# Performance work log

Measured on AMD Instinct MI355X. Metric: run time of the kernel, lower is better.

The kernel has to match this reference:

```python
import jax, jax.numpy as jnp
import numpy as np

NUM_EMB = 256
EMB_DIM = 128
COMMIT_COST = 0.25


def setup_inputs() -> dict:
    key = jax.random.key(0)
    k1, k2 = jax.random.split(key)
    z = jax.random.normal(k1, (64, EMB_DIM, 64, 64), dtype=jnp.float32)
    # codebook initialized uniform(-1/num_embeddings, 1/num_embeddings)
    emb = jax.random.uniform(k2, (NUM_EMB, EMB_DIM), dtype=jnp.float32,
                             minval=-1.0 / NUM_EMB, maxval=1.0 / NUM_EMB)
    return {"z": z, "emb": emb}


def reference(z, emb):
    B, C, H, W = z.shape
    # [B, C, H, W] -> [B*H*W, C]
    z_flat = jnp.transpose(z, (0, 2, 3, 1)).reshape(-1, C)
    # squared L2 distances to each code: ||z||^2 - 2 z.e + ||e||^2, shape [N, K]
    d = (jnp.sum(z_flat * z_flat, axis=1, keepdims=True)
         - 2.0 * jnp.einsum('nc,kc->nk', z_flat, emb)
         + jnp.sum(emb * emb, axis=1))
    idx = jnp.argmin(d, axis=1)  # [N]
    # gather codes, back to NCHW
    quantized = emb[idx].reshape(B, H, W, C)
    quantized = jnp.transpose(quantized, (0, 3, 1, 2))
    commitment_loss = COMMIT_COST * jnp.mean(
        (jax.lax.stop_gradient(quantized) - z) ** 2)
    codebook_loss = jnp.mean((quantized - jax.lax.stop_gradient(z)) ** 2)
    # straight-through estimator
    quantized_ste = z + jax.lax.stop_gradient(quantized - z)
    return (quantized_ste, idx.reshape(B, H, W), commitment_loss, codebook_loss)
```

## Files before the change

kernel.cpp:

```cpp
#include <hip/hip_runtime.h>

#define K_EMB   256
#define C_DIM   128
#define HW      4096
#define NPOS    262144
#define Q_ELEMS 33554432
#define IDX_OFF Q_ELEMS
#define LOSS_OFF (Q_ELEMS + NPOS)

#define BLKP 64
#define TK   32
#define NQ   8
#define NTHR 512

#define WS_ENORM 0
#define WS_ACC   256
#define WS_EMBT  512
#define WS_NEED_FULL  ((WS_EMBT + C_DIM * K_EMB) * 4)

__global__ __launch_bounds__(K_EMB) void vq_transpose(const float* __restrict__ emb,
                                                      float* __restrict__ ws,
                                                      int use_embT) {
    const int c = blockIdx.x, k = threadIdx.x;
    if (use_embT) ws[WS_EMBT + c * K_EMB + k] = emb[k * C_DIM + c];
    if (c == 0 && k == 0) ws[WS_ACC] = 0.f;
}

__global__ __launch_bounds__(K_EMB) void vq_enorm(const float* __restrict__ emb,
                                                  float* __restrict__ ws) {
    const int k = threadIdx.x;
    const float4* __restrict__ er = reinterpret_cast<const float4*>(emb + k * C_DIM);
    float s = 0.f;
    #pragma unroll
    for (int j = 0; j < C_DIM / 4; ++j) {
        float4 v = er[j];
        s = fmaf(v.x, v.x, s);
        s = fmaf(v.y, v.y, s);
        s = fmaf(v.z, v.z, s);
        s = fmaf(v.w, v.w, s);
    }
    ws[WS_ENORM + k] = s;
}

template <int UT>
__global__ __launch_bounds__(NTHR, 4) void vq_main(const float* __restrict__ z,
                                                   const float* __restrict__ emb,
                                                   const float* __restrict__ ws,
                                                   float* __restrict__ out,
                                                   float* __restrict__ loss_acc) {
    __shared__ float zlds[C_DIM * BLKP];
    __shared__ float sh_best[NQ * BLKP];
    __shared__ int   sh_bidx[NQ * BLKP];

    const int t    = threadIdx.x;
    const int lane = t & 63;
    const int kq   = t >> 6;
    const int blk  = blockIdx.x;
    const int b    = blk >> 6;
    const int hw0  = (blk & 63) * BLKP;
    const size_t zoff = (size_t)b * (C_DIM * HW) + hw0;
    const float* __restrict__ zsrc = z + zoff;

    {
        const float4* __restrict__ zs4 = reinterpret_cast<const float4*>(zsrc);
        float4* __restrict__ zl4 = reinterpret_cast<float4*>(zlds);
        #pragma unroll
        for (int j = 0; j < (C_DIM * BLKP / 4) / NTHR; ++j) {
            const int i4 = t + j * NTHR;
            const int c  = i4 >> 4;
            const int p4 = i4 & 15;
            zl4[i4] = zs4[(size_t)c * (HW / 4) + p4];
        }
    }
    __syncthreads();

    const float* __restrict__ embT  = ws + WS_EMBT;
    const float* __restrict__ enorm = ws + WS_ENORM;

    const int kbase = __builtin_amdgcn_readfirstlane(kq * TK);

    float acc[TK];
    #pragma unroll
    for (int j = 0; j < TK; ++j) acc[j] = 0.f;
    float znorm = 0.f;

    #pragma unroll 2
    for (int c = 0; c < C_DIM; ++c) {
        const float zc = zlds[c * BLKP + lane];
        znorm = fmaf(zc, zc, znorm);
        if (UT) {
            const float* __restrict__ ep = embT + c * K_EMB + kbase;
            #pragma unroll
            for (int j = 0; j < TK; ++j)
                acc[j] = fmaf(zc, ep[j], acc[j]);
        } else {
            #pragma unroll
            for (int j = 0; j < TK; ++j)
                acc[j] = fmaf(zc, emb[(kbase + j) * C_DIM + c], acc[j]);
        }
    }

    float best = 3.402823466e38f;
    int   bidx = 0;
    #pragma unroll
    for (int j = 0; j < TK; ++j) {
        const float d = (znorm - 2.0f * acc[j]) + enorm[kbase + j];
        if (d < best) { best = d; bidx = kbase + j; }
    }

    sh_best[t] = best;
    sh_bidx[t] = bidx;
    __syncthreads();

    if (t < BLKP) {
        const int p = t;
        float bb = sh_best[p];
        int   bi = sh_bidx[p];
        #pragma unroll
        for (int q = 1; q < NQ; ++q) {
            const float bq = sh_best[q * BLKP + p];
            const int   iq = sh_bidx[q * BLKP + p];
            if (bq < bb) { bb = bq; bi = iq; }
        }
        const int fin = bi;
        const int pos = blk * BLKP + p;
        __builtin_nontemporal_store((float)fin, &out[IDX_OFF + pos]);

        float lsum = 0.f;
        float* qp = out + zoff + p;
        const float4* __restrict__ er =
            reinterpret_cast<const float4*>(emb + fin * C_DIM);
        #pragma unroll 4
        for (int j = 0; j < C_DIM / 4; ++j) {
            const float4 ev = er[j];
            const int c0 = j * 4;
            const float z0 = zlds[(c0 + 0) * BLKP + p];
            const float z1 = zlds[(c0 + 1) * BLKP + p];
            const float z2 = zlds[(c0 + 2) * BLKP + p];
            const float z3 = zlds[(c0 + 3) * BLKP + p];
            const float d0 = ev.x - z0, d1 = ev.y - z1;
            const float d2 = ev.z - z2, d3 = ev.w - z3;
            lsum = fmaf(d0, d0, lsum);
            lsum = fmaf(d1, d1, lsum);
            lsum = fmaf(d2, d2, lsum);
            lsum = fmaf(d3, d3, lsum);
            __builtin_nontemporal_store(z0 + d0, &qp[(size_t)(c0 + 0) * HW]);
            __builtin_nontemporal_store(z1 + d1, &qp[(size_t)(c0 + 1) * HW]);
            __builtin_nontemporal_store(z2 + d2, &qp[(size_t)(c0 + 2) * HW]);
            __builtin_nontemporal_store(z3 + d3, &qp[(size_t)(c0 + 3) * HW]);
        }

        #pragma unroll
        for (int off = 32; off > 0; off >>= 1)
            lsum += __shfl_down(lsum, off, 64);
        if (p == 0) atomicAdd(loss_acc, lsum);
    }
}

__global__ void vq_finalize(const float* __restrict__ loss_acc,
                            float* __restrict__ out_losses) {
    float S = loss_acc[0];
    float mean = S / (float)Q_ELEMS;
    out_losses[0] = 0.25f * mean;
    out_losses[1] = mean;
}

extern "C" void kernel_launch(void* const* d_in, const int* in_sizes, int n_in,
                              void* d_out, int out_size, void* d_ws, size_t ws_size,
                              hipStream_t stream) {
    const float* z   = (const float*)d_in[0];
    const float* emb = (const float*)d_in[1];
    float* out = (float*)d_out;
    float* ws  = (float*)d_ws;

    int use_embT = (ws_size >= (size_t)WS_NEED_FULL) ? 1 : 0;

    vq_transpose<<<C_DIM, K_EMB, 0, stream>>>(emb, ws, use_embT);
    vq_enorm<<<1, K_EMB, 0, stream>>>(emb, ws);
    if (use_embT)
        vq_main<1><<<NPOS / BLKP, NTHR, 0, stream>>>(z, emb, ws, out, ws + WS_ACC);
    else
        vq_main<0><<<NPOS / BLKP, NTHR, 0, stream>>>(z, emb, ws, out, ws + WS_ACC);
    vq_finalize<<<1, 1, 0, stream>>>(ws + WS_ACC, out + LOSS_OFF);
}
```

Before: 391.1 us.

## Register-tile distance GEMM as 4x8 position-by-code blocks with LDS argmin reduction

Replaces the one-position-per-thread, 32-codes-per-thread layout with a 4 positions × 8 codes register tile per thread. Each thread now does float4 LDS reads of z and float4 global reads of the transposed codebook, so every loaded value feeds more FMAs. The z norm is computed once per position by 64 threads instead of redundantly in the inner loop, and the code norms are staged in LDS. Partial argmins from 32 code groups go through LDS with packed byte indices and are reduced there. This adds an extra barrier and a longer final reduction loop (32 groups instead of 8).

```diff
diff --git a/kernel.cpp b/kernel.cpp
--- a/kernel.cpp
+++ b/kernel.cpp
@@ -9,9 +9,10 @@
 #define LOSS_OFF (Q_ELEMS + NPOS)
 
 #define BLKP 64
-#define TK   32
-#define NQ   8
 #define NTHR 512
+#define TM   4
+#define TN   8
+#define NKG  32
 
 #define WS_ENORM 0
 #define WS_ACC   256
@@ -49,17 +50,24 @@
                                                    float* __restrict__ out,
                                                    float* __restrict__ loss_acc) {
     __shared__ float zlds[C_DIM * BLKP];
-    __shared__ float sh_best[NQ * BLKP];
-    __shared__ int   sh_bidx[NQ * BLKP];
-
-    const int t    = threadIdx.x;
-    const int lane = t & 63;
-    const int kq   = t >> 6;
-    const int blk  = blockIdx.x;
-    const int b    = blk >> 6;
-    const int hw0  = (blk & 63) * BLKP;
+    __shared__ float shz[BLKP];
+    __shared__ float shen[K_EMB];
+    __shared__ float shpb[NKG * BLKP];
+    __shared__ unsigned int shpi[NKG * BLKP / 4];
+
+    const int t   = threadIdx.x;
+    const int pg  = t & 15;
+    const int p0  = pg * 4;
+    const int kg  = t >> 4;
+    const int k0  = kg * TN;
+    const int blk = blockIdx.x;
+    const int b   = blk >> 6;
+    const int hw0 = (blk & 63) * BLKP;
     const size_t zoff = (size_t)b * (C_DIM * HW) + hw0;
     const float* __restrict__ zsrc = z + zoff;
+
+    const float* __restrict__ embT    = ws + WS_EMBT;
+    const float* __restrict__ enorm_g = ws + WS_ENORM;
 
     {
         const float4* __restrict__ zs4 = reinterpret_cast<const float4*>(zsrc);
@@ -71,55 +79,80 @@
             const int p4 = i4 & 15;
             zl4[i4] = zs4[(size_t)c * (HW / 4) + p4];
         }
+        if (t < K_EMB) shen[t] = enorm_g[t];
     }
     __syncthreads();
 
-    const float* __restrict__ embT  = ws + WS_EMBT;
-    const float* __restrict__ enorm = ws + WS_ENORM;
-
-    const int kbase = __builtin_amdgcn_readfirstlane(kq * TK);
-
-    float acc[TK];
+    if (t < BLKP) {
+        float zn = 0.f;
+        #pragma unroll 8
+        for (int c = 0; c < C_DIM; ++c) {
+            const float zc = zlds[c * BLKP + t];
+            zn = fmaf(zc, zc, zn);
+        }
+        shz[t] = zn;
+    }
+
+    float acc[TM][TN];
     #pragma unroll
-    for (int j = 0; j < TK; ++j) acc[j] = 0.f;
-    float znorm = 0.f;
-
-    #pragma unroll 2
+    for (int i = 0; i < TM; ++i)
+        #pragma unroll
+        for (int j = 0; j < TN; ++j) acc[i][j] = 0.f;
+
+    #pragma unroll 4
     for (int c = 0; c < C_DIM; ++c) {
-        const float zc = zlds[c * BLKP + lane];
-        znorm = fmaf(zc, zc, znorm);
+        const float4 zv = *reinterpret_cast<const float4*>(&zlds[c * BLKP + p0]);
+        float ev[TN];
         if (UT) {
-            const float* __restrict__ ep = embT + c * K_EMB + kbase;
-            #pragma unroll
-            for (int j = 0; j < TK; ++j)
-                acc[j] = fmaf(zc, ep[j], acc[j]);
+            const float4* __restrict__ ep =
+                reinterpret_cast<const float4*>(embT + c * K_EMB + k0);
+            const float4 e0 = ep[0];
+            const float4 e1 = ep[1];
+            ev[0] = e0.x; ev[1] = e0.y; ev[2] = e0.z; ev[3] = e0.w;
+            ev[4] = e1.x; ev[5] = e1.y; ev[6] = e1.z; ev[7] = e1.w;
         } else {
             #pragma unroll
-            for (int j = 0; j < TK; ++j)
-                acc[j] = fmaf(zc, emb[(kbase + j) * C_DIM + c], acc[j]);
-        }
-    }
-
-    float best = 3.402823466e38f;
-    int   bidx = 0;
-    #pragma unroll
-    for (int j = 0; j < TK; ++j) {
-        const float d = (znorm - 2.0f * acc[j]) + enorm[kbase + j];
-        if (d < best) { best = d; bidx = kbase + j; }
-    }
-
-    sh_best[t] = best;
-    sh_bidx[t] = bidx;
+            for (int j = 0; j < TN; ++j) ev[j] = emb[(k0 + j) * C_DIM + c];
+        }
+        const float zz[TM] = {zv.x, zv.y, zv.z, zv.w};
+        #pragma unroll
+        for (int i = 0; i < TM; ++i)
+            #pragma unroll
+            for (int j = 0; j < TN; ++j)
+                acc[i][j] = fmaf(zz[i], ev[j], acc[i][j]);
+    }
+    __syncthreads();
+
+    {
+        float pb[TM];
+        int   pi[TM];
+        #pragma unroll
+        for (int i = 0; i < TM; ++i) {
+            const float zn = shz[p0 + i];
+            float best = 3.402823466e38f;
+            int   bi = 0;
+            #pragma unroll
+            for (int j = 0; j < TN; ++j) {
+                const float d = (zn - 2.0f * acc[i][j]) + shen[k0 + j];
+                if (d < best) { best = d; bi = k0 + j; }
+            }
+            pb[i] = best; pi[i] = bi;
+        }
+        *reinterpret_cast<float4*>(&shpb[kg * BLKP + p0]) =
+            make_float4(pb[0], pb[1], pb[2], pb[3]);
+        shpi[kg * 16 + pg] = (unsigned)(pi[0] & 255) | ((unsigned)(pi[1] & 255) << 8)
+                           | ((unsigned)(pi[2] & 255) << 16) | ((unsigned)(pi[3] & 255) << 24);
+    }
     __syncthreads();
 
     if (t < BLKP) {
         const int p = t;
-        float bb = sh_best[p];
-        int   bi = sh_bidx[p];
-        #pragma unroll
-        for (int q = 1; q < NQ; ++q) {
-            const float bq = sh_best[q * BLKP + p];
-            const int   iq = sh_bidx[q * BLKP + p];
+        float bb = shpb[p];
+        int   bi = (shpi[p >> 2] >> ((p & 3) * 8)) & 255;
+        #pragma unroll 4
+        for (int g = 1; g < NKG; ++g) {
+            const float bq = shpb[g * BLKP + p];
+            const int   iq = (shpi[g * 16 + (p >> 2)] >> ((p & 3) * 8)) & 255;
             if (bq < bb) { bb = bq; bi = iq; }
         }
         const int fin = bi;
```

Measured after the change: 456.8 us. 16.8% more time.

## Stage transposed codebook chunks in LDS with register-prefetched double buffering

Applied to the files above, without the earlier changes.

The distance loop now reads the transposed codebook from shared memory in 32-channel chunks instead of from global memory. The next chunk is prefetched into registers while the current one is consumed, then written to LDS between barriers. This aims to cut global and scalar-cache traffic for codebook reads. In exchange it adds 32KB of LDS per block, which lowers occupancy, plus extra barriers.

```diff
diff --git a/kernel.cpp b/kernel.cpp
--- a/kernel.cpp
+++ b/kernel.cpp
@@ -12,6 +12,8 @@
 #define TK   32
 #define NQ   8
 #define NTHR 512
+#define CC   32
+#define NCHUNK (C_DIM / CC)
 
 #define WS_ENORM 0
 #define WS_ACC   256
@@ -49,6 +51,7 @@
                                                    float* __restrict__ out,
                                                    float* __restrict__ loss_acc) {
     __shared__ float zlds[C_DIM * BLKP];
+    __shared__ float embc[CC * K_EMB];
     __shared__ float sh_best[NQ * BLKP];
     __shared__ int   sh_bidx[NQ * BLKP];
 
@@ -61,6 +64,9 @@
     const size_t zoff = (size_t)b * (C_DIM * HW) + hw0;
     const float* __restrict__ zsrc = z + zoff;
 
+    const float* __restrict__ embT  = ws + WS_EMBT;
+    const float* __restrict__ enorm = ws + WS_ENORM;
+
     {
         const float4* __restrict__ zs4 = reinterpret_cast<const float4*>(zsrc);
         float4* __restrict__ zl4 = reinterpret_cast<float4*>(zlds);
@@ -71,11 +77,15 @@
             const int p4 = i4 & 15;
             zl4[i4] = zs4[(size_t)c * (HW / 4) + p4];
         }
+        if (UT) {
+            const float4* __restrict__ es4 = reinterpret_cast<const float4*>(embT);
+            float4* __restrict__ el4 = reinterpret_cast<float4*>(embc);
+            #pragma unroll
+            for (int i = 0; i < 4; ++i)
+                el4[t + i * NTHR] = es4[t + i * NTHR];
+        }
     }
     __syncthreads();
-
-    const float* __restrict__ embT  = ws + WS_EMBT;
-    const float* __restrict__ enorm = ws + WS_ENORM;
 
     const int kbase = __builtin_amdgcn_readfirstlane(kq * TK);
 
@@ -84,16 +94,45 @@
     for (int j = 0; j < TK; ++j) acc[j] = 0.f;
     float znorm = 0.f;
 
-    #pragma unroll 2
-    for (int c = 0; c < C_DIM; ++c) {
-        const float zc = zlds[c * BLKP + lane];
-        znorm = fmaf(zc, zc, znorm);
-        if (UT) {
-            const float* __restrict__ ep = embT + c * K_EMB + kbase;
-            #pragma unroll
-            for (int j = 0; j < TK; ++j)
-                acc[j] = fmaf(zc, ep[j], acc[j]);
-        } else {
+    if (UT) {
+        float4 pf[4];
+        #pragma unroll
+        for (int ch = 0; ch < NCHUNK; ++ch) {
+            if (ch + 1 < NCHUNK) {
+                const float4* __restrict__ ns4 =
+                    reinterpret_cast<const float4*>(embT + (ch + 1) * CC * K_EMB);
+                #pragma unroll
+                for (int i = 0; i < 4; ++i) pf[i] = ns4[t + i * NTHR];
+            }
+            #pragma unroll 2
+            for (int c = 0; c < CC; ++c) {
+                const int cg = ch * CC + c;
+                const float zc = zlds[cg * BLKP + lane];
+                znorm = fmaf(zc, zc, znorm);
+                const float4* __restrict__ ep4 =
+                    reinterpret_cast<const float4*>(&embc[c * K_EMB + kbase]);
+                #pragma unroll
+                for (int j4 = 0; j4 < TK / 4; ++j4) {
+                    const float4 e = ep4[j4];
+                    acc[j4 * 4 + 0] = fmaf(zc, e.x, acc[j4 * 4 + 0]);
+                    acc[j4 * 4 + 1] = fmaf(zc, e.y, acc[j4 * 4 + 1]);
+                    acc[j4 * 4 + 2] = fmaf(zc, e.z, acc[j4 * 4 + 2]);
+                    acc[j4 * 4 + 3] = fmaf(zc, e.w, acc[j4 * 4 + 3]);
+                }
+            }
+            if (ch + 1 < NCHUNK) {
+                __syncthreads();
+                float4* __restrict__ el4 = reinterpret_cast<float4*>(embc);
+                #pragma unroll
+                for (int i = 0; i < 4; ++i) el4[t + i * NTHR] = pf[i];
+                __syncthreads();
+            }
+        }
+    } else {
+        #pragma unroll 2
+        for (int c = 0; c < C_DIM; ++c) {
+            const float zc = zlds[c * BLKP + lane];
+            znorm = fmaf(zc, zc, znorm);
             #pragma unroll
             for (int j = 0; j < TK; ++j)
                 acc[j] = fmaf(zc, emb[(kbase + j) * C_DIM + c], acc[j]);
```

New measurement: 519.0 us. 1.33x slower.
